# Performance work log

Measured on AMD Instinct MI355X. Metric: run time of the kernel, lower is better.

Reference implementation:

```python
import jax, jax.numpy as jnp
import numpy as np

N_NODES = 50000
N_GRAPHS = 256
IN_DIM = 128
HID = 128
N_LAYERS = 3
N_EDGES = 800000


def setup_inputs() -> dict:
    key = jax.random.key(0)
    ks = jax.random.split(key, 16)
    x = jax.random.normal(ks[0], (N_NODES, IN_DIM), dtype=jnp.float32)
    edge_index = jax.random.randint(ks[1], (2, N_EDGES), 0, N_NODES, dtype=jnp.int64)
    batch = jnp.sort(jax.random.randint(ks[2], (N_NODES,), 0, N_GRAPHS, dtype=jnp.int64))
    inp = {"x": x, "edge_index": edge_index, "batch": batch}
    # SAGEConv params per PyG: lin_l (bias) applied to mean-aggregated neighbors,
    # lin_r (no bias) applied to the root node feature.
    dims = [(IN_DIM, HID)] + [(HID, HID)] * (N_LAYERS - 1)
    for i, (din, dout) in enumerate(dims):
        s = 1.0 / np.sqrt(din)
        inp[f"Wl{i}"] = jax.random.uniform(ks[3 + 3 * i], (din, dout), jnp.float32, -s, s)
        inp[f"bl{i}"] = jax.random.uniform(ks[4 + 3 * i], (dout,), jnp.float32, -s, s)
        inp[f"Wr{i}"] = jax.random.uniform(ks[5 + 3 * i], (din, dout), jnp.float32, -s, s)
    return inp


def _sage_conv(x, src, dst, Wl, bl, Wr):
    # mean aggregation of source-node messages into destination nodes
    msg = x[src]                                               # [E, d] gather
    agg = jax.ops.segment_sum(msg, dst, num_segments=N_NODES)  # [N, d] scatter-add
    deg = jax.ops.segment_sum(jnp.ones((src.shape[0], 1), x.dtype), dst,
                              num_segments=N_NODES)
    agg = agg / jnp.maximum(deg, 1.0)
    return agg @ Wl + bl + x @ Wr


def reference(x, edge_index, batch, Wl0, bl0, Wr0, Wl1, bl1, Wr1, Wl2, bl2, Wr2):
    src, dst = edge_index[0], edge_index[1]
    params = [(Wl0, bl0, Wr0), (Wl1, bl1, Wr1), (Wl2, bl2, Wr2)]
    h = x
    for Wl, bl, Wr in params:
        h = jax.nn.relu(_sage_conv(h, src, dst, Wl, bl, Wr))
        # dropout is a no-op in eval mode
    # meanmax readout over graph ids
    cnt = jax.ops.segment_sum(jnp.ones((h.shape[0], 1), h.dtype), batch,
                              num_segments=N_GRAPHS)
    g_mean = jax.ops.segment_sum(h, batch, num_segments=N_GRAPHS) / jnp.maximum(cnt, 1.0)
    g_max = jax.ops.segment_max(h, batch, num_segments=N_GRAPHS)
    g_max = jnp.where(jnp.isfinite(g_max), g_max, 0.0)  # empty graphs -> 0
    return jnp.concatenate([g_mean, g_max], axis=-1)    # [G, 2*HID]
```

## Files before the change

### kernel.cpp

```cpp
#include <hip/hip_runtime.h>
#include <hip/hip_bf16.h>
#include <stdint.h>

#define N_NODES  50000
#define N_GRAPHS 256
#define DIM      128
#define N_EDGES  800000
#define K2       256
#define N_STRIPS (N_NODES / 16)
#define PAD_CAP  64
#define NBUCKET  196
#define NCHUNK   256
#define CHUNK    3125

typedef __attribute__((ext_vector_type(8))) short  short8;
typedef __attribute__((ext_vector_type(4))) float  floatx4;

__device__ __forceinline__ ushort f2bf(float f) {
    union { float f; uint32_t u; } c; c.f = f;
    uint32_t u = c.u;
    return (ushort)((u + 0x7fffu + ((u >> 16) & 1u)) >> 16);
}
__device__ __forceinline__ float bf2f(ushort b) {
    union { uint32_t u; float f; } c; c.u = ((uint32_t)b) << 16;
    return c.f;
}

__global__ __launch_bounds__(256) void k_convert_x(const float* __restrict__ x,
                                                   ushort* __restrict__ xb) {
    int i = blockIdx.x * 256 + threadIdx.x;
    const int n4 = N_NODES * DIM / 4;
    if (i < n4) {
        float4 v = ((const float4*)x)[i];
        uint32_t lo = (uint32_t)f2bf(v.x) | ((uint32_t)f2bf(v.y) << 16);
        uint32_t hi = (uint32_t)f2bf(v.z) | ((uint32_t)f2bf(v.w) << 16);
        ((uint2*)xb)[i] = make_uint2(lo, hi);
    }
}

__global__ __launch_bounds__(256) void k_prep_w_all(const float* __restrict__ Wl0, const float* __restrict__ Wr0,
                                                    const float* __restrict__ Wl1, const float* __restrict__ Wr1,
                                                    const float* __restrict__ Wl2, const float* __restrict__ Wr2,
                                                    ushort* __restrict__ Wt) {
    int i = blockIdx.x * 256 + threadIdx.x;
    if (i < 3 * DIM * K2) {
        int layer = i / (DIM * K2);
        int j = i % (DIM * K2);
        int n = j / K2, k = j % K2;
        const float* Wl = (layer == 0) ? Wl0 : (layer == 1) ? Wl1 : Wl2;
        const float* Wr = (layer == 0) ? Wr0 : (layer == 1) ? Wr1 : Wr2;
        float v = (k < DIM) ? Wl[k * DIM + n] : Wr[(k - DIM) * DIM + n];
        Wt[i] = f2bf(v);
    }
}

__global__ __launch_bounds__(256) void k_hist(const int* __restrict__ dst,
                                              int* __restrict__ counts) {
    __shared__ int hist[NBUCKET];
    int t = threadIdx.x, b = blockIdx.x;
    if (t < NBUCKET) hist[t] = 0;
    __syncthreads();
    const int e0 = b * CHUNK;
    for (int i = t; i < CHUNK; i += 256)
        atomicAdd(&hist[dst[e0 + i] >> 8], 1);
    __syncthreads();
    if (t < NBUCKET) counts[b * NBUCKET + t] = hist[t];
}

__global__ __launch_bounds__(256) void k_scan_col(const int* __restrict__ counts,
                                                  int* __restrict__ off,
                                                  int* __restrict__ total) {
    __shared__ int buf[256];
    int t = threadIdx.x, j = blockIdx.x;
    int v = counts[t * NBUCKET + j];
    buf[t] = v;
    __syncthreads();
    #pragma unroll
    for (int d = 1; d < 256; d <<= 1) {
        int x = (t >= d) ? buf[t - d] : 0;
        __syncthreads();
        buf[t] += x;
        __syncthreads();
    }
    off[t * NBUCKET + j] = buf[t] - v;
    if (t == 255) total[j] = buf[255];
}

__global__ __launch_bounds__(256) void k_scan_total(const int* __restrict__ total,
                                                    int* __restrict__ basep) {
    __shared__ int buf[256];
    int t = threadIdx.x;
    int v = (t < NBUCKET) ? total[t] : 0;
    buf[t] = v;
    __syncthreads();
    #pragma unroll
    for (int d = 1; d < 256; d <<= 1) {
        int x = (t >= d) ? buf[t - d] : 0;
        __syncthreads();
        buf[t] += x;
        __syncthreads();
    }
    if (t < NBUCKET) basep[t] = buf[t] - v;
}

__global__ __launch_bounds__(256) void k_scatter(const int* __restrict__ src,
                                                 const int* __restrict__ dst,
                                                 const int* __restrict__ off,
                                                 const int* __restrict__ basep,
                                                 uint32_t* __restrict__ ebuf) {
    __shared__ int cur[NBUCKET];
    int t = threadIdx.x, b = blockIdx.x;
    if (t < NBUCKET) cur[t] = off[b * NBUCKET + t] + basep[t];
    __syncthreads();
    const int e0 = b * CHUNK;
    for (int i = t; i < CHUNK; i += 256) {
        int d = dst[e0 + i];
        int s = src[e0 + i];
        int p = atomicAdd(&cur[d >> 8], 1);
        ebuf[p] = ((uint32_t)(d & 255) << 16) | (uint32_t)s;
    }
}

__global__ __launch_bounds__(256) void k_build(const uint32_t* __restrict__ ebuf,
                                               const int* __restrict__ total,
                                               const int* __restrict__ basep,
                                               int* __restrict__ padded,
                                               int* __restrict__ cnt) {
    __shared__ int lcnt[256];
    int t = threadIdx.x, j = blockIdx.x;
    lcnt[t] = 0;
    __syncthreads();
    int b0 = basep[j], tot = total[j];
    for (int i = t; i < tot; i += 256) {
        uint32_t v = ebuf[b0 + i];
        int dl = (int)(v >> 16);
        int s  = (int)(v & 0xffffu);
        int p  = atomicAdd(&lcnt[dl], 1);
        if (p < PAD_CAP) padded[((size_t)j * 256 + dl) * PAD_CAP + p] = s;
    }
    __syncthreads();
    int node = j * 256 + t;
    if (node < N_NODES) cnt[node] = lcnt[t];
}

__global__ __launch_bounds__(256) void k_sort_adj(int* __restrict__ padded,
                                                  const int* __restrict__ cnt) {
    int wid  = threadIdx.x >> 6;
    int lane = threadIdx.x & 63;
    int node = blockIdx.x * 4 + wid;
    if (node >= N_NODES) return;
    int deg = cnt[node];
    int m   = deg < PAD_CAP ? deg : PAD_CAP;
    int* lst = padded + (size_t)node * PAD_CAP;
    int v = (lane < m) ? lst[lane] : 0x7fffffff;
    #pragma unroll
    for (int k = 2; k <= 64; k <<= 1) {
        #pragma unroll
        for (int j = k >> 1; j > 0; j >>= 1) {
            int other  = __shfl_xor(v, j, 64);
            bool down  = (lane & k) != 0;
            bool lower = (lane & j) == 0;
            v = (lower ^ down) ? min(v, other) : max(v, other);
        }
    }
    if (lane < m) lst[lane] = v;
}

__global__ __launch_bounds__(256) void k_gbounds(const int* __restrict__ batch,
                                                 int* __restrict__ gstart,
                                                 int* __restrict__ gend) {
    int i = blockIdx.x * 256 + threadIdx.x;
    if (i >= N_NODES) return;
    int g = batch[i];
    if (i == 0) gstart[g] = 0;
    int gn = (i + 1 < N_NODES) ? batch[i + 1] : -1;
    if (gn != g) {
        gend[g] = i + 1;
        if (gn >= 0) gstart[gn] = i + 1;
    }
}

template <bool OUT_F32>
__global__ __launch_bounds__(256) void k_layer(const ushort* __restrict__ h_in,
                                               const int* __restrict__ padded,
                                               const int* __restrict__ cnt,
                                               const ushort* __restrict__ Wt,
                                               const float* __restrict__ bias,
                                               ushort* __restrict__ out_bf,
                                               float* __restrict__ out_f) {
    __shared__ ushort sAgg[16 * DIM];
    __shared__ int    sIdx[16 * PAD_CAP];
    __shared__ int    sCnt[16];
    __shared__ int    sChl[4][17];
    __shared__ int    sNch[4];

    int t    = threadIdx.x;
    int wid  = t >> 6;
    int lane = t & 63;
    int r0   = blockIdx.x * 16;
    const uint32_t* hw = (const uint32_t*)h_in;

    ((int4*)sIdx)[t] = ((const int4*)(padded + (size_t)r0 * PAD_CAP))[t];
    if (t < 16) sCnt[t] = cnt[r0 + t];
    __syncthreads();

    if (lane == 0) {
        int n = 0;
        #pragma unroll
        for (int q = 0; q < 4; ++q) {
            int m = min(sCnt[wid * 4 + q], PAD_CAP);
            for (int e0 = 0; e0 < m; e0 += 16)
                sChl[wid][n++] = q | (e0 << 8);
        }
        sNch[wid] = n;
    }
    #pragma unroll
    for (int q = 0; q < 4; ++q) {
        int node = wid * 4 + q;
        if (sCnt[node] == 0) ((uint32_t*)(sAgg + node * DIM))[lane] = 0u;
    }
    int nch = sNch[wid];

    float ax[4] = {0.f, 0.f, 0.f, 0.f};
    float ay[4] = {0.f, 0.f, 0.f, 0.f};
    uint32_t va[16], vb[16];

    auto issue = [&](int ci, uint32_t (&v)[16]) {
        int ch   = sChl[wid][ci];
        int q    = ch & 255, e0 = ch >> 8;
        int node = wid * 4 + q;
        int m    = min(sCnt[node], PAD_CAP);
        const int* lst = sIdx + node * PAD_CAP;
        #pragma unroll
        for (int k = 0; k < 16; ++k) {
            int ek = e0 + k;
            int id = lst[ek < m ? ek : m - 1];
            v[k] = hw[(size_t)id * 64 + lane];
        }
    };
    auto consume = [&](int ci, uint32_t (&v)[16], bool isLast) {
        int ch   = sChl[wid][ci];
        int q    = ch & 255, e0 = ch >> 8;
        int node = wid * 4 + q;
        int deg  = sCnt[node];
        int m    = min(deg, PAD_CAP);
        #pragma unroll
        for (int k = 0; k < 16; ++k) {
            uint32_t w = (e0 + k < m) ? v[k] : 0u;
            ax[k & 3] += __uint_as_float(w << 16);
            ay[k & 3] += __uint_as_float(w & 0xffff0000u);
        }
        bool lastOfNode = isLast || ((sChl[wid][ci + 1] & 255) != q);
        if (lastOfNode) {
            float axs = (ax[0] + ax[1]) + (ax[2] + ax[3]);
            float ays = (ay[0] + ay[1]) + (ay[2] + ay[3]);
            float inv = 1.0f / (float)(deg > 0 ? deg : 1);
            uint32_t o = (uint32_t)f2bf(axs * inv) | ((uint32_t)f2bf(ays * inv) << 16);
            ((uint32_t*)(sAgg + node * DIM))[lane] = o;
            #pragma unroll
            for (int j = 0; j < 4; ++j) { ax[j] = 0.f; ay[j] = 0.f; }
        }
    };

    if (nch > 0) {
        issue(0, va);
        int i = 0;
        while (true) {
            bool hasB = (i + 1) < nch;
            if (hasB) issue(i + 1, vb);
            consume(i, va, !hasB);
            if (!hasB) break;
            bool hasA = (i + 2) < nch;
            if (hasA) issue(i + 2, va);
            consume(i + 1, vb, !hasA);
            if (!hasA) break;
            i += 2;
        }
    }
    __syncthreads();

    int row  = lane & 15;
    int quad = lane >> 4;
    short8 a[8];
    const ushort* srow = sAgg + row * DIM + quad * 8;
    #pragma unroll
    for (int ks = 0; ks < 4; ++ks) a[ks] = *(const short8*)(srow + ks * 32);
    const ushort* hrow = h_in + (size_t)(r0 + row) * DIM + quad * 8;
    #pragma unroll
    for (int ks = 0; ks < 4; ++ks) a[4 + ks] = *(const short8*)(hrow + ks * 32);

    #pragma unroll
    for (int c = 0; c < 2; ++c) {
        int ct  = wid * 2 + c;
        int col = ct * 16 + row;
        const ushort* wrow = Wt + (size_t)col * K2 + quad * 8;
        floatx4 acc = {0.f, 0.f, 0.f, 0.f};
        #pragma unroll
        for (int ks = 0; ks < 8; ++ks) {
            short8 b = *(const short8*)(wrow + ks * 32);
            acc = __builtin_amdgcn_mfma_f32_16x16x32_bf16(a[ks], b, acc, 0, 0, 0);
        }
        float bv = bias[col];
        #pragma unroll
        for (int r = 0; r < 4; ++r) {
            int m = r0 + quad * 4 + r;
            float v = acc[r] + bv;
            v = v > 0.f ? v : 0.f;
            if (OUT_F32) out_f[(size_t)m * DIM + col] = v;
            else         out_bf[(size_t)m * DIM + col] = f2bf(v);
        }
    }
}

__global__ __launch_bounds__(128) void k_readout(const float* __restrict__ h,
                                                 const int* __restrict__ batch,
                                                 float* __restrict__ out) {
    int d  = threadIdx.x;
    int n0 = blockIdx.x * 128;
    int n1 = min(n0 + 128, N_NODES);
    int cur = -1; float sum = 0.f, mx = 0.f;
    for (int i = n0; i < n1; ++i) {
        int g = batch[i];
        if (g != cur) {
            if (cur >= 0) {
                atomicAdd(&out[cur * 2 * DIM + d], sum);
                atomicMax((int*)&out[cur * 2 * DIM + DIM + d], __float_as_int(mx));
            }
            cur = g; sum = 0.f; mx = 0.f;
        }
        float v = h[(size_t)i * DIM + d];
        sum += v; mx = fmaxf(mx, v);
    }
    if (cur >= 0) {
        atomicAdd(&out[cur * 2 * DIM + d], sum);
        atomicMax((int*)&out[cur * 2 * DIM + DIM + d], __float_as_int(mx));
    }
}

__global__ __launch_bounds__(256) void k_finalize(float* __restrict__ out,
                                                  const int* __restrict__ gstart,
                                                  const int* __restrict__ gend) {
    int i = blockIdx.x * 256 + threadIdx.x;
    if (i < N_GRAPHS * DIM) {
        int g = i / DIM, d = i % DIM;
        int c = gend[g] - gstart[g];
        out[g * 2 * DIM + d] /= (float)(c > 0 ? c : 1);
    }
}

extern "C" void kernel_launch(void* const* d_in, const int* in_sizes, int n_in,
                              void* d_out, int out_size, void* d_ws, size_t ws_size,
                              hipStream_t stream) {
    const float* x     = (const float*)d_in[0];
    const int*   ei    = (const int*)d_in[1];
    const int*   src   = ei;
    const int*   dst   = ei + N_EDGES;
    const int*   batch = (const int*)d_in[2];
    const float* Wl[3] = {(const float*)d_in[3], (const float*)d_in[6], (const float*)d_in[9]};
    const float* bl[3] = {(const float*)d_in[4], (const float*)d_in[7], (const float*)d_in[10]};
    const float* Wr[3] = {(const float*)d_in[5], (const float*)d_in[8], (const float*)d_in[11]};
    float* out = (float*)d_out;

    char* base = (char*)d_ws;
    size_t o = 0;
    auto alloc = [&](size_t b) -> char* {
        char* p = base + o;
        o = (o + b + 255) & ~(size_t)255;
        return p;
    };
    int*     gstart = (int*)alloc((size_t)N_GRAPHS * 4);
    int*     gend   = (int*)alloc((size_t)N_GRAPHS * 4);
    size_t   zero_bytes = o;
    int*     cnt    = (int*)alloc((size_t)N_NODES * 4);
    int*     counts = (int*)alloc((size_t)NCHUNK * NBUCKET * 4);
    int*     offs   = (int*)alloc((size_t)NCHUNK * NBUCKET * 4);
    int*     total  = (int*)alloc((size_t)NBUCKET * 4);
    int*     basep  = (int*)alloc((size_t)NBUCKET * 4);
    uint32_t* ebuf  = (uint32_t*)alloc((size_t)N_EDGES * 4);
    int*     padded = (int*)alloc((size_t)N_NODES * PAD_CAP * 4);
    ushort*  xb     = (ushort*)alloc((size_t)N_NODES * DIM * 2);
    ushort*  ha     = (ushort*)alloc((size_t)N_NODES * DIM * 2);
    ushort*  hb     = (ushort*)alloc((size_t)N_NODES * DIM * 2);
    float*   h3     = (float*)alloc((size_t)N_NODES * DIM * 4);
    ushort*  Wt     = (ushort*)alloc((size_t)3 * DIM * K2 * 2);
    (void)ws_size; (void)n_in; (void)in_sizes;

    hipMemsetAsync(base, 0, zero_bytes, stream);
    hipMemsetAsync(d_out, 0, (size_t)out_size * 4, stream);

    k_convert_x<<<(N_NODES * DIM / 4 + 255) / 256, 256, 0, stream>>>(x, xb);
    k_prep_w_all<<<(3 * DIM * K2 + 255) / 256, 256, 0, stream>>>(
        Wl[0], Wr[0], Wl[1], Wr[1], Wl[2], Wr[2], Wt);

    k_hist<<<NCHUNK, 256, 0, stream>>>(dst, counts);
    k_scan_col<<<NBUCKET, 256, 0, stream>>>(counts, offs, total);
    k_scan_total<<<1, 256, 0, stream>>>(total, basep);
    k_scatter<<<NCHUNK, 256, 0, stream>>>(src, dst, offs, basep, ebuf);
    k_build<<<NBUCKET, 256, 0, stream>>>(ebuf, total, basep, padded, cnt);
    k_sort_adj<<<(N_NODES + 3) / 4, 256, 0, stream>>>(padded, cnt);
    k_gbounds<<<(N_NODES + 255) / 256, 256, 0, stream>>>(batch, gstart, gend);

    k_layer<false><<<N_STRIPS, 256, 0, stream>>>(xb, padded, cnt, Wt,              bl[0], ha, nullptr);
    k_layer<false><<<N_STRIPS, 256, 0, stream>>>(ha, padded, cnt, Wt + DIM * K2,   bl[1], hb, nullptr);
    k_layer<true ><<<N_STRIPS, 256, 0, stream>>>(hb, padded, cnt, Wt + 2 * DIM * K2, bl[2], nullptr, h3);

    k_readout<<<(N_NODES + 127) / 128, 128, 0, stream>>>(h3, batch, out);
    k_finalize<<<(N_GRAPHS * DIM + 255) / 256, 256, 0, stream>>>(out, gstart, gend);
}
```

Before: 348.0 us.

## Gather neighbor rows via async global-to-LDS loads and shrink readout row chunks

The neighbor-aggregation gather now uses global_load_lds, copying 16-byte row pieces straight into a per-wave double-buffered LDS pool instead of holding 32 registers of loaded values. Manual vmcnt waits with scheduling barriers overlap the next chunk's loads with accumulation of the current one. The goal is to cut register pressure and keep more gather bytes in flight. The cost is extra LDS traffic and about 32 KB more shared memory per block, which may lower occupancy. Separately, the readout kernel handles 32 rows per block instead of 128, giving more blocks and more parallelism at the price of more atomics.

```diff
diff --git a/kernel.cpp b/kernel.cpp
--- a/kernel.cpp
+++ b/kernel.cpp
@@ -12,9 +12,15 @@
 #define NBUCKET  196
 #define NCHUNK   256
 #define CHUNK    3125
+#define RO_ROWS  32
 
 typedef __attribute__((ext_vector_type(8))) short  short8;
 typedef __attribute__((ext_vector_type(4))) float  floatx4;
+
+#define WAITVM4() do { asm volatile("s_waitcnt vmcnt(4)" ::: "memory"); \
+                       __builtin_amdgcn_sched_barrier(0); } while (0)
+#define WAITVM0() do { asm volatile("s_waitcnt vmcnt(0)" ::: "memory"); \
+                       __builtin_amdgcn_sched_barrier(0); } while (0)
 
 __device__ __forceinline__ ushort f2bf(float f) {
     union { float f; uint32_t u; } c; c.f = f;
@@ -188,17 +194,17 @@
                                                const float* __restrict__ bias,
                                                ushort* __restrict__ out_bf,
                                                float* __restrict__ out_f) {
-    __shared__ ushort sAgg[16 * DIM];
-    __shared__ int    sIdx[16 * PAD_CAP];
-    __shared__ int    sCnt[16];
-    __shared__ int    sChl[4][17];
-    __shared__ int    sNch[4];
+    __shared__ uint32_t sPool[4 * 2 * 16 * 64];
+    __shared__ ushort   sAgg[16 * DIM];
+    __shared__ int      sIdx[16 * PAD_CAP];
+    __shared__ int      sCnt[16];
+    __shared__ int      sChl[4][17];
+    __shared__ int      sNch[4];
 
     int t    = threadIdx.x;
     int wid  = t >> 6;
     int lane = t & 63;
     int r0   = blockIdx.x * 16;
-    const uint32_t* hw = (const uint32_t*)h_in;
 
     ((int4*)sIdx)[t] = ((const int4*)(padded + (size_t)r0 * PAD_CAP))[t];
     if (t < 16) sCnt[t] = cnt[r0 + t];
@@ -221,60 +227,60 @@
     }
     int nch = sNch[wid];
 
-    float ax[4] = {0.f, 0.f, 0.f, 0.f};
-    float ay[4] = {0.f, 0.f, 0.f, 0.f};
-    uint32_t va[16], vb[16];
-
-    auto issue = [&](int ci, uint32_t (&v)[16]) {
-        int ch   = sChl[wid][ci];
-        int q    = ch & 255, e0 = ch >> 8;
-        int node = wid * 4 + q;
-        int m    = min(sCnt[node], PAD_CAP);
-        const int* lst = sIdx + node * PAD_CAP;
-        #pragma unroll
-        for (int k = 0; k < 16; ++k) {
-            int ek = e0 + k;
-            int id = lst[ek < m ? ek : m - 1];
-            v[k] = hw[(size_t)id * 64 + lane];
-        }
-    };
-    auto consume = [&](int ci, uint32_t (&v)[16], bool isLast) {
-        int ch   = sChl[wid][ci];
-        int q    = ch & 255, e0 = ch >> 8;
-        int node = wid * 4 + q;
-        int deg  = sCnt[node];
-        int m    = min(deg, PAD_CAP);
-        #pragma unroll
-        for (int k = 0; k < 16; ++k) {
-            uint32_t w = (e0 + k < m) ? v[k] : 0u;
-            ax[k & 3] += __uint_as_float(w << 16);
-            ay[k & 3] += __uint_as_float(w & 0xffff0000u);
-        }
-        bool lastOfNode = isLast || ((sChl[wid][ci + 1] & 255) != q);
-        if (lastOfNode) {
-            float axs = (ax[0] + ax[1]) + (ax[2] + ax[3]);
-            float ays = (ay[0] + ay[1]) + (ay[2] + ay[3]);
-            float inv = 1.0f / (float)(deg > 0 ? deg : 1);
-            uint32_t o = (uint32_t)f2bf(axs * inv) | ((uint32_t)f2bf(ays * inv) << 16);
-            ((uint32_t*)(sAgg + node * DIM))[lane] = o;
+    {
+        float ax[4] = {0.f, 0.f, 0.f, 0.f};
+        float ay[4] = {0.f, 0.f, 0.f, 0.f};
+        int   sub   = lane >> 4;
+        int   boff  = (lane & 15) << 4;
+
+        auto stage = [&](int cj) {
+            int ch = sChl[wid][cj];
+            int q = ch & 255, e0 = ch >> 8;
+            int node = wid * 4 + q;
+            int m = min(sCnt[node], PAD_CAP);
+            const int* lst = sIdx + node * PAD_CAP;
+            uint32_t* db = sPool + ((wid * 2 + (cj & 1)) << 10);
             #pragma unroll
-            for (int j = 0; j < 4; ++j) { ax[j] = 0.f; ay[j] = 0.f; }
-        }
-    };
-
-    if (nch > 0) {
-        issue(0, va);
-        int i = 0;
-        while (true) {
-            bool hasB = (i + 1) < nch;
-            if (hasB) issue(i + 1, vb);
-            consume(i, va, !hasB);
-            if (!hasB) break;
-            bool hasA = (i + 2) < nch;
-            if (hasA) issue(i + 2, va);
-            consume(i + 1, vb, !hasA);
-            if (!hasA) break;
-            i += 2;
+            for (int g = 0; g < 4; ++g) {
+                int ek = e0 + g * 4 + sub;
+                int id = lst[ek < m ? ek : m - 1];
+                const char* gp = (const char*)h_in + ((size_t)id << 8) + boff;
+                __builtin_amdgcn_global_load_lds(
+                    (const __attribute__((address_space(1))) uint32_t*)gp,
+                    (__attribute__((address_space(3))) uint32_t*)(db + g * 256),
+                    16, 0, 0);
+            }
+        };
+
+        if (nch > 0) {
+            stage(0);
+            for (int ci = 0; ci < nch; ++ci) {
+                if (ci + 1 < nch) { stage(ci + 1); WAITVM4(); }
+                else              { WAITVM0(); }
+                int ch = sChl[wid][ci];
+                int q = ch & 255, e0 = ch >> 8;
+                int node = wid * 4 + q;
+                int deg = sCnt[node];
+                int m = min(deg, PAD_CAP);
+                const uint32_t* bp = sPool + ((wid * 2 + (ci & 1)) << 10);
+                #pragma unroll
+                for (int k = 0; k < 16; ++k) {
+                    uint32_t w = bp[k * 64 + lane];
+                    if (e0 + k >= m) w = 0u;
+                    ax[k & 3] += __uint_as_float(w << 16);
+                    ay[k & 3] += __uint_as_float(w & 0xffff0000u);
+                }
+                bool last = (ci + 1 >= nch) || ((sChl[wid][ci + 1] & 255) != q);
+                if (last) {
+                    float axs = (ax[0] + ax[1]) + (ax[2] + ax[3]);
+                    float ays = (ay[0] + ay[1]) + (ay[2] + ay[3]);
+                    float inv = 1.0f / (float)(deg > 0 ? deg : 1);
+                    uint32_t o = (uint32_t)f2bf(axs * inv) | ((uint32_t)f2bf(ays * inv) << 16);
+                    ((uint32_t*)(sAgg + node * DIM))[lane] = o;
+                    #pragma unroll
+                    for (int j = 0; j < 4; ++j) { ax[j] = 0.f; ay[j] = 0.f; }
+                }
+            }
         }
     }
     __syncthreads();
@@ -316,8 +322,8 @@
                                                  const int* __restrict__ batch,
                                                  float* __restrict__ out) {
     int d  = threadIdx.x;
-    int n0 = blockIdx.x * 128;
-    int n1 = min(n0 + 128, N_NODES);
+    int n0 = blockIdx.x * RO_ROWS;
+    int n1 = min(n0 + RO_ROWS, N_NODES);
     int cur = -1; float sum = 0.f, mx = 0.f;
     for (int i = n0; i < n1; ++i) {
         int g = batch[i];
@@ -404,6 +410,6 @@
     k_layer<false><<<N_STRIPS, 256, 0, stream>>>(ha, padded, cnt, Wt + DIM * K2,   bl[1], hb, nullptr);
     k_layer<true ><<<N_STRIPS, 256, 0, stream>>>(hb, padded, cnt, Wt + 2 * DIM * K2, bl[2], nullptr, h3);
 
-    k_readout<<<(N_NODES + 127) / 128, 128, 0, stream>>>(h3, batch, out);
+    k_readout<<<(N_NODES + RO_ROWS - 1) / RO_ROWS, 128, 0, stream>>>(h3, batch, out);
     k_finalize<<<(N_GRAPHS * DIM + 255) / 256, 256, 0, stream>>>(out, gstart, gend);
 }
```

New measurement: 356.3 us. +2.4%, slower.
